# Performance work log

Hardware: AMD Instinct MI355X
Metric: run time of the kernel (lower is better)

## Reference

```python
import jax, jax.numpy as jnp
import numpy as np

FACTOR = 3   # ProbAttention factor hardcoded in Informer.__init__
N_HEADS = 8


def _ln(x, g, b, eps=1e-5):
    m = x.mean(-1, keepdims=True)
    v = ((x - m) ** 2).mean(-1, keepdims=True)
    return (x - m) / jnp.sqrt(v + eps) * g + b


def _pos_emb(L, d_model):
    # standard fixed sinusoidal positional embedding (Informer PositionalEmbedding)
    pos = np.arange(L, dtype=np.float32)[:, None]
    div = np.exp(np.arange(0, d_model, 2, dtype=np.float32) * (-np.log(10000.0) / d_model))
    pe = np.zeros((L, d_model), np.float32)
    pe[:, 0::2] = np.sin(pos * div)
    pe[:, 1::2] = np.cos(pos * div)
    return jnp.asarray(pe)


def _prob_attention(q, k, v, rng_key):
    # q,k,v: [B, L, H, D]; mask_flag=False, scale=None -> 1/sqrt(D)
    B, L, H, D = q.shape
    Q = q.transpose(0, 2, 1, 3)
    K = k.transpose(0, 2, 1, 3)
    V = v.transpose(0, 2, 1, 3)
    L_Q = L_K = L
    U_part = min(FACTOR * int(np.ceil(np.log(L_K))), L_K)   # sampled keys per query
    u = min(FACTOR * int(np.ceil(np.log(L_Q))), L_Q)        # top queries kept
    # sample keys (shared across batch/heads, as in torch.randint(L_K,(L_Q,sample_k)))
    idx_sample = jax.random.randint(rng_key, (L_Q, U_part), 0, L_K)
    K_sample = K[:, :, idx_sample, :]                        # [B,H,L_Q,U_part,D]
    QK_sample = jnp.einsum('bhld,bhlsd->bhls', Q, K_sample)  # [B,H,L_Q,U_part]
    M = QK_sample.max(-1) - QK_sample.sum(-1) / L_K          # sparsity measure [B,H,L_Q]
    _, idx_top = jax.lax.top_k(M, u)                         # [B,H,u]
    Q_reduce = jnp.take_along_axis(Q, idx_top[..., None], axis=2)          # [B,H,u,D]
    scores = jnp.einsum('bhud,bhkd->bhuk', Q_reduce, K) / jnp.sqrt(jnp.float32(D))
    attn = jax.nn.softmax(scores, axis=-1)
    upd = jnp.einsum('bhuk,bhkd->bhud', attn, V)             # [B,H,u,D]
    # initial context = mean over values (mask_flag=False), overwrite at top queries
    ctx = jnp.broadcast_to(V.mean(axis=2, keepdims=True), (B, H, L_Q, D))
    bI = jnp.arange(B)[:, None, None]
    hI = jnp.arange(H)[None, :, None]
    ctx = ctx.at[bI, hI, idx_top].set(upd)
    return ctx.transpose(0, 2, 1, 3).reshape(B, L, H * D)


def _forward(x, time_features, g_in, b_in, W_tok, W_time, b_time,
             Wq, bq, Wk, bk, Wv, bv, Wo, bo, W1, b1, W2, b2,
             g1, be1, g2, be2, g_enc, b_enc, W_pre, b_pre, W_fc, b_fc):
    B, L, _ = x.shape
    d_model = W_tok.shape[-1]
    H = N_HEADS
    D = d_model // H
    x = _ln(x, g_in, b_in)                                   # input_norm over enc_in
    # DataEmbedding: circular Conv1d(k=3) token emb + positional + timeF linear
    xp = jnp.pad(x, ((0, 0), (1, 1), (0, 0)), mode='wrap')
    tok = jax.lax.conv_general_dilated(xp, W_tok, (1,), 'VALID',
                                       dimension_numbers=('NWC', 'WIO', 'NWC'))
    h = tok + _pos_emb(L, d_model)[None] + time_features @ W_time.T + b_time
    key = jax.random.key(42)
    for i in range(Wq.shape[0]):                              # e_layers (small, fixed)
        q = (h @ Wq[i].T + bq[i]).reshape(B, L, H, D)
        k = (h @ Wk[i].T + bk[i]).reshape(B, L, H, D)
        v = (h @ Wv[i].T + bv[i]).reshape(B, L, H, D)
        attn_out = _prob_attention(q, k, v, jax.random.fold_in(key, i))
        h = h + attn_out @ Wo[i].T + bo[i]
        h = _ln(h, g1[i], be1[i])
        y = jax.nn.relu(h @ W1[i].T + b1[i]) @ W2[i].T + b2[i]  # 1x1 convs == linears
        h = _ln(h + y, g2[i], be2[i])
    h = _ln(h, g_enc, b_enc)
    last = h[:, -1, :]
    return jax.nn.relu(last @ W_pre.T + b_pre) @ W_fc.T + b_fc


def setup_inputs() -> dict:
    key = jax.random.key(0)
    B, L, C_IN, DM, DFF, E = 8, 2048, 32, 512, 2048, 2
    ks = iter(jax.random.split(key, 48))

    def p(shape, s=0.02):
        return jax.random.normal(next(ks), shape, jnp.float32) * s

    return {
        'x': jax.random.normal(next(ks), (B, L, C_IN), jnp.float32),
        'time_features': jax.random.uniform(next(ks), (B, L, 4), jnp.float32),
        'g_in': jnp.ones((C_IN,), jnp.float32), 'b_in': jnp.zeros((C_IN,), jnp.float32),
        'W_tok': p((3, C_IN, DM)),
        'W_time': p((DM, 4)), 'b_time': jnp.zeros((DM,), jnp.float32),
        'Wq': p((E, DM, DM)), 'bq': jnp.zeros((E, DM), jnp.float32),
        'Wk': p((E, DM, DM)), 'bk': jnp.zeros((E, DM), jnp.float32),
        'Wv': p((E, DM, DM)), 'bv': jnp.zeros((E, DM), jnp.float32),
        'Wo': p((E, DM, DM)), 'bo': jnp.zeros((E, DM), jnp.float32),
        'W1': p((E, DFF, DM)), 'b1': jnp.zeros((E, DFF), jnp.float32),
        'W2': p((E, DM, DFF)), 'b2': jnp.zeros((E, DM), jnp.float32),
        'g1': jnp.ones((E, DM), jnp.float32), 'be1': jnp.zeros((E, DM), jnp.float32),
        'g2': jnp.ones((E, DM), jnp.float32), 'be2': jnp.zeros((E, DM), jnp.float32),
        'g_enc': jnp.ones((DM,), jnp.float32), 'b_enc': jnp.zeros((DM,), jnp.float32),
        'W_pre': p((DM // 2, DM)), 'b_pre': jnp.zeros((DM // 2,), jnp.float32),
        'W_fc': p((1, DM // 2)), 'b_fc': jnp.zeros((1,), jnp.float32),
    }


def reference(x, time_features, g_in, b_in, W_tok, W_time, b_time,
              Wq, bq, Wk, bk, Wv, bv, Wo, bo, W1, b1, W2, b2,
              g1, be1, g2, be2, g_enc, b_enc, W_pre, b_pre, W_fc, b_fc):
    return _forward(x, time_features, g_in, b_in, W_tok, W_time, b_time,
                    Wq, bq, Wk, bk, Wv, bv, Wo, bo, W1, b1, W2, b2,
                    g1, be1, g2, be2, g_enc, b_enc, W_pre, b_pre, W_fc, b_fc)
```

## Files before the change

### kernel.cpp

```cpp
#include <hip/hip_runtime.h>
#include <math.h>

#define BATCH 8
#define SEQ   2048
#define TOK   (BATCH*SEQ)
#define CIN   32
#define DM    512
#define DFF   2048
#define NH    8
#define HD    64
#define NSAMP 24
#define NTOP  24
#define EPS   1e-5f
#define QKVLD 1536

typedef unsigned int u32;
typedef unsigned short u16;
typedef unsigned long long u64;
typedef __attribute__((ext_vector_type(8))) short short8;
typedef __attribute__((ext_vector_type(4))) short short4v;
typedef __attribute__((ext_vector_type(4))) float floatx4;

__device__ __forceinline__ void async16(const void* g, void* l) {
    __builtin_amdgcn_global_load_lds((const __attribute__((address_space(1))) u32*)g,
                                     (__attribute__((address_space(3))) u32*)l, 16, 0, 0);
}
__device__ __forceinline__ u16 bf16rn(float f) {
    u32 u = __float_as_uint(f);
    return (u16)((u + 0x7fffu + ((u >> 16) & 1u)) >> 16);
}
__device__ __forceinline__ void sep_store(u16* base, size_t row, int ld2, int j, float v) {
    u16 hb = bf16rn(v);
    float r = v - __uint_as_float((u32)hb << 16);
    size_t o = row * (size_t)ld2 + (size_t)((j >> 3) << 4) + (j & 7);
    base[o] = hb;
    base[o + 8] = bf16rn(r);
}
__device__ __forceinline__ float sep_load(const u16* base, size_t row, int ld2, int j) {
    size_t o = row * (size_t)ld2 + (size_t)((j >> 3) << 4) + (j & 7);
    return __uint_as_float((u32)base[o] << 16) + __uint_as_float((u32)base[o + 8] << 16);
}
__device__ __forceinline__ float hl2f(u16 h, u16 l) {
    return __uint_as_float((u32)h << 16) + __uint_as_float((u32)l << 16);
}

__device__ __forceinline__ void tf_round(unsigned &x0, unsigned &x1, int r) {
    x0 += x1;
    x1 = (x1 << r) | (x1 >> (32 - r));
    x1 ^= x0;
}
__device__ __forceinline__ void threefry(unsigned k0, unsigned k1,
                                         unsigned c0, unsigned c1,
                                         unsigned &o0, unsigned &o1) {
    unsigned ks0 = k0, ks1 = k1, ks2 = k0 ^ k1 ^ 0x1BD11BDAu;
    unsigned x0 = c0 + ks0, x1 = c1 + ks1;
    tf_round(x0,x1,13); tf_round(x0,x1,15); tf_round(x0,x1,26); tf_round(x0,x1,6);
    x0 += ks1; x1 += ks2 + 1u;
    tf_round(x0,x1,17); tf_round(x0,x1,29); tf_round(x0,x1,16); tf_round(x0,x1,24);
    x0 += ks2; x1 += ks0 + 2u;
    tf_round(x0,x1,13); tf_round(x0,x1,15); tf_round(x0,x1,26); tf_round(x0,x1,6);
    x0 += ks0; x1 += ks1 + 3u;
    tf_round(x0,x1,17); tf_round(x0,x1,29); tf_round(x0,x1,16); tf_round(x0,x1,24);
    x0 += ks1; x1 += ks2 + 4u;
    tf_round(x0,x1,13); tf_round(x0,x1,15); tf_round(x0,x1,26); tf_round(x0,x1,6);
    x0 += ks2; x1 += ks0 + 5u;
    o0 = x0; o1 = x1;
}

__global__ void sample_kernel(int* __restrict__ idx_sample) {
    const int HALF = (SEQ * NSAMP) / 2;
    int p = blockIdx.x * blockDim.x + threadIdx.x;
    int li = blockIdx.y;
    if (p >= HALF) return;
    unsigned f0, f1;
    threefry(0u, 42u, 0u, (unsigned)li, f0, f1);
    unsigned a0, a1, b0, b1;
    threefry(f0, f1, 0u, 2u, a0, a1);
    threefry(f0, f1, 1u, 3u, b0, b1);
    unsigned o0, o1;
    threefry(a1, b1, (unsigned)p, (unsigned)(p + HALF), o0, o1);
    idx_sample[li * SEQ * NSAMP + p]        = (int)(o0 & (SEQ - 1));
    idx_sample[li * SEQ * NSAMP + p + HALF] = (int)(o1 & (SEQ - 1));
}

__global__ __launch_bounds__(256) void ln_in_kernel(const float* __restrict__ x,
        const float* __restrict__ g, const float* __restrict__ b,
        float* __restrict__ out) {
    int t = blockIdx.x * blockDim.x + threadIdx.x;
    if (t >= TOK) return;
    const float* xr = x + (size_t)t * CIN;
    float vals[CIN];
    float s = 0.f;
#pragma unroll
    for (int c = 0; c < CIN; c++) { vals[c] = xr[c]; s += vals[c]; }
    float m = s * (1.f / CIN);
    float v = 0.f;
#pragma unroll
    for (int c = 0; c < CIN; c++) { float d = vals[c] - m; v += d * d; }
    v *= (1.f / CIN);
    float inv = rsqrtf(v + EPS);
    float* orow = out + (size_t)t * CIN;
#pragma unroll
    for (int c = 0; c < CIN; c++) orow[c] = (vals[c] - m) * inv * g[c] + b[c];
}

__global__ __launch_bounds__(128) void im2col_kernel(const float* __restrict__ xln,
        u16* __restrict__ a) {
    int t = blockIdx.x;
    int j = threadIdx.x;
    if (j >= 96) return;
    int b = t >> 11, l = t & 2047;
    int w = j >> 5, c = j & 31;
    int lw = (l - 1 + w + SEQ) & 2047;
    sep_store(a, (size_t)t, 192, j, xln[(((size_t)b << 11) | lw) * CIN + c]);
}

__global__ __launch_bounds__(256) void wtok_split(const float* __restrict__ Wtok,
        u16* __restrict__ wt) {
    int e = blockIdx.x * 256 + threadIdx.x;
    int o = e / 96, j = e % 96;
    sep_store(wt, (size_t)o, 192, j, Wtok[(size_t)j * DM + o]);
}

__global__ __launch_bounds__(256) void pe_kernel(float* __restrict__ pe) {
    int e = blockIdx.x * 256 + threadIdx.x;
    int l = e >> 9, o = e & 511;
    const float c1 = -0.017988946039016f;
    int i2 = o & ~1;
    float div = expf((float)i2 * c1);
    float arg = (float)l * div;
    pe[e] = (o & 1) ? cosf(arg) : sinf(arg);
}

__global__ __launch_bounds__(256) void rsd_kernel(const float* __restrict__ pe,
        const float* __restrict__ tfeat, const float* __restrict__ Wtime,
        u16* __restrict__ rsd) {
    int t = blockIdx.x, tid = threadIdx.x;
    int l = t & 2047;
    float t0 = tfeat[(size_t)t * 4], t1 = tfeat[(size_t)t * 4 + 1];
    float t2 = tfeat[(size_t)t * 4 + 2], t3 = tfeat[(size_t)t * 4 + 3];
    for (int o = tid; o < DM; o += 256) {
        float v = pe[l * DM + o]
            + t0 * Wtime[o * 4] + t1 * Wtime[o * 4 + 1]
            + t2 * Wtime[o * 4 + 2] + t3 * Wtime[o * 4 + 3];
        sep_store(rsd, (size_t)t, 1024, o, v);
    }
}

__global__ __launch_bounds__(256) void split_weights(const float* __restrict__ Wq,
        const float* __restrict__ Wk, const float* __restrict__ Wv,
        const float* __restrict__ Wo, const float* __restrict__ W1,
        const float* __restrict__ W2, u16* __restrict__ out,
        const float* __restrict__ bq, const float* __restrict__ bk,
        const float* __restrict__ bv, float* __restrict__ bqkv) {
    int i = blockIdx.x * 256 + threadIdx.x;
    if (i < 1536)
        bqkv[i] = (i < 512) ? bq[i] : (i < 1024) ? bk[i - 512] : bv[i - 1024];
    if (i < 1048576) {
        const float* src = (i < 262144) ? Wq : (i < 524288) ? Wk : (i < 786432) ? Wv : Wo;
        int off = i & 262143;
        size_t base = (size_t)(i >> 18) * 524288;
        sep_store(out + base, (size_t)(off >> 9), 1024, off & 511, src[off]);
    } else if (i < 2097152) {
        int off = i - 1048576;
        sep_store(out + 2097152, (size_t)(off >> 9), 1024, off & 511, W1[off]);
    } else {
        int off = i - 2097152;
        sep_store(out + 4194304, (size_t)(off >> 11), 4096, off & 2047, W2[off]);
    }
}

template<bool RELU, bool RESP, bool OUTP, bool OUTB>
__global__ __launch_bounds__(256, 2) void gemm_pp(const u16* __restrict__ Ap,
        const u16* __restrict__ Wp, const float* __restrict__ bias,
        const u16* __restrict__ RsdS, float* __restrict__ Cf, u16* __restrict__ Cp,
        int ldc, int K, int lda) {
    __shared__ alignas(16) u16 At[2][8192];
    __shared__ alignas(16) u16 Wt[2][8192];
    const int tid = threadIdx.x;
    int linear = blockIdx.y * gridDim.x + blockIdx.x;
    int xcd = linear & 7, sseq = linear >> 3;
    int mper = gridDim.y >> 3;
    int mt = xcd * mper + (sseq % mper);
    int nt = sseq / mper;
    const int m0 = mt * 128, n0 = nt * 128;
    const int lane = tid & 63, wv = tid >> 6;
    const int wm = wv >> 1, wn = wv & 1;
    const int fr = lane & 15, q = lane >> 4;

    floatx4 acc[4][4] = {};

    const int r0 = tid >> 3;
    const int gc = (tid & 7) ^ (r0 & 7);
    const u16* abase = Ap + (size_t)(m0 + r0) * (2 * lda) + gc * 8;
    const u16* wbase = Wp + (size_t)(n0 + r0) * (2 * K) + gc * 8;
    const size_t astep = (size_t)32 * 2 * lda;
    const size_t wstep = (size_t)32 * 2 * K;
    const int doff = tid * 16;
    const int nk = K >> 5;

    const int cph = ((q << 1) ^ (fr & 7)) << 3;
    const int cpl = ((q << 1) ^ (fr & 7) ^ 1) << 3;

#pragma unroll
    for (int i = 0; i < 4; i++) {
        async16(abase + i * astep, (char*)At[0] + doff + i * 4096);
        async16(wbase + i * wstep, (char*)Wt[0] + doff + i * 4096);
    }

    for (int k = 0; k < nk; k++) {
        const int b = k & 1;
        __syncthreads();
        if (k + 1 < nk) {
            int k2 = (k + 1) << 6;
#pragma unroll
            for (int i = 0; i < 4; i++) {
                async16(abase + k2 + i * astep, (char*)At[b ^ 1] + doff + i * 4096);
                async16(wbase + k2 + i * wstep, (char*)Wt[b ^ 1] + doff + i * 4096);
            }
        }
        short8 ah[4], al[4];
#pragma unroll
        for (int mi = 0; mi < 4; mi++) {
            int r = wm * 64 + mi * 16 + fr;
            ah[mi] = *(const short8*)&At[b][r * 64 + cph];
            al[mi] = *(const short8*)&At[b][r * 64 + cpl];
        }
#pragma unroll
        for (int ni = 0; ni < 4; ni++) {
            int r = wn * 64 + ni * 16 + fr;
            short8 wh8 = *(const short8*)&Wt[b][r * 64 + cph];
            short8 wl8 = *(const short8*)&Wt[b][r * 64 + cpl];
#pragma unroll
            for (int mi = 0; mi < 4; mi++) {
                acc[mi][ni] = __builtin_amdgcn_mfma_f32_16x16x32_bf16(ah[mi], wh8, acc[mi][ni], 0, 0, 0);
                acc[mi][ni] = __builtin_amdgcn_mfma_f32_16x16x32_bf16(ah[mi], wl8, acc[mi][ni], 0, 0, 0);
                acc[mi][ni] = __builtin_amdgcn_mfma_f32_16x16x32_bf16(al[mi], wh8, acc[mi][ni], 0, 0, 0);
            }
        }
    }
#pragma unroll
    for (int ni = 0; ni < 4; ni++) {
        int col = n0 + wn * 64 + ni * 16 + fr;
        float bv = bias[col];
#pragma unroll
        for (int mi = 0; mi < 4; mi++) {
            int row = m0 + wm * 64 + mi * 16 + q * 4;
#pragma unroll
            for (int r = 0; r < 4; r++) {
                float v = acc[mi][ni][r] + bv;
                if (RESP) v += sep_load(RsdS, (size_t)(row + r), 2 * ldc, col);
                if (RELU) v = fmaxf(v, 0.f);
                if (OUTP)      sep_store(Cp, (size_t)(row + r), 2 * ldc, col, v);
                else if (OUTB) Cp[(size_t)(row + r) * ldc + col] = bf16rn(v);
                else           Cf[(size_t)(row + r) * ldc + col] = v;
            }
        }
    }
}

template<int CFG, bool RELU, bool RESP, bool OUTP, bool OUTB>
__global__ __launch_bounds__(512, 2) void gemm8(const u16* __restrict__ Ap,
        const u16* __restrict__ Wp, const float* __restrict__ bias,
        const u16* __restrict__ RsdS, float* __restrict__ Cf, u16* __restrict__ Cp,
        int ldc, int K, int lda) {
    constexpr int BM = CFG ? 256 : 128;
    constexpr int BN = CFG ? 128 : 256;
    constexpr int NA = BM / 64;
    constexpr int NW = BN / 64;
    __shared__ alignas(16) u16 As[3][BM * 64];
    __shared__ alignas(16) u16 Ws[3][BN * 64];
    const int tid = threadIdx.x;
    int linear = blockIdx.y * gridDim.x + blockIdx.x;
    int xcd = linear & 7, sseq = linear >> 3;
    int mper = gridDim.y >> 3;
    int mt = xcd * mper + (sseq % mper);
    int nt = sseq / mper;
    const int m0 = mt * BM, n0 = nt * BN;
    const int lane = tid & 63, wv = tid >> 6;
    const int wm = CFG ? (wv >> 1) : (wv >> 2);
    const int wn = CFG ? (wv & 1) : (wv & 3);
    const int fr = lane & 15, q = lane >> 4;

    floatx4 acc[4][4] = {};

    const int r0 = tid >> 3;
    const int gc = (tid & 7) ^ (r0 & 7);
    const u16* abase = Ap + (size_t)(m0 + r0) * (2 * lda) + gc * 8;
    const u16* wbase = Wp + (size_t)(n0 + r0) * (2 * K) + gc * 8;
    const size_t astep = (size_t)64 * 2 * lda;
    const size_t wstep = (size_t)64 * 2 * K;
    const int doff = tid * 16;
    const int nk = K >> 5;

    const int cph = ((q << 1) ^ (fr & 7)) << 3;
    const int cpl = cph ^ 8;

#pragma unroll
    for (int i = 0; i < NA; i++) async16(abase + i * astep, (char*)As[0] + doff + i * 8192);
#pragma unroll
    for (int i = 0; i < NW; i++) async16(wbase + i * wstep, (char*)Ws[0] + doff + i * 8192);
#pragma unroll
    for (int i = 0; i < NA; i++) async16(abase + 64 + i * astep, (char*)As[1] + doff + i * 8192);
#pragma unroll
    for (int i = 0; i < NW; i++) async16(wbase + 64 + i * wstep, (char*)Ws[1] + doff + i * 8192);
    asm volatile("s_waitcnt vmcnt(6)" ::: "memory");
    __builtin_amdgcn_s_barrier();

    int cur = 0;
    for (int k = 0; k < nk; k++) {
        const u16* Ab = As[cur];
        const u16* Wb = Ws[cur];
        int nxt = cur + 2; if (nxt >= 3) nxt -= 3;
        const bool stage = (k + 2) < nk;
        const int ko = (k + 2) << 6;

        short8 ah[4], al[4];
#pragma unroll
        for (int mi = 0; mi < 4; mi++) {
            int r = wm * 64 + mi * 16 + fr;
            ah[mi] = *(const short8*)&Ab[r * 64 + cph];
            al[mi] = *(const short8*)&Ab[r * 64 + cpl];
        }
        short8 wh, wl;
        {
            int r = wn * 64 + fr;
            wh = *(const short8*)&Wb[r * 64 + cph];
            wl = *(const short8*)&Wb[r * 64 + cpl];
        }
        if (stage) {
#pragma unroll
            for (int i = 0; i < NA; i++)
                async16(abase + ko + i * astep, (char*)As[nxt] + doff + i * 8192);
        }
        __builtin_amdgcn_s_barrier();
        asm volatile("s_waitcnt lgkmcnt(0)" ::: "memory");
        __builtin_amdgcn_sched_barrier(0);
        __builtin_amdgcn_s_setprio(1);
#pragma unroll
        for (int mi = 0; mi < 4; mi++) {
            acc[mi][0] = __builtin_amdgcn_mfma_f32_16x16x32_bf16(ah[mi], wh, acc[mi][0], 0, 0, 0);
            acc[mi][0] = __builtin_amdgcn_mfma_f32_16x16x32_bf16(ah[mi], wl, acc[mi][0], 0, 0, 0);
            acc[mi][0] = __builtin_amdgcn_mfma_f32_16x16x32_bf16(al[mi], wh, acc[mi][0], 0, 0, 0);
        }
        __builtin_amdgcn_s_setprio(0);
        __builtin_amdgcn_s_barrier();

#pragma unroll
        for (int ni = 1; ni < 4; ni++) {
            int r = wn * 64 + ni * 16 + fr;
            wh = *(const short8*)&Wb[r * 64 + cph];
            wl = *(const short8*)&Wb[r * 64 + cpl];
            if (stage) {
                if (ni == 1) {
#pragma unroll
                    for (int i = 0; i < NW / 2; i++)
                        async16(wbase + ko + i * wstep, (char*)Ws[nxt] + doff + i * 8192);
                } else if (ni == 2) {
#pragma unroll
                    for (int i = NW / 2; i < NW; i++)
                        async16(wbase + ko + i * wstep, (char*)Ws[nxt] + doff + i * 8192);
                }
            }
            __builtin_amdgcn_s_barrier();
            asm volatile("s_waitcnt lgkmcnt(0)" ::: "memory");
            __builtin_amdgcn_sched_barrier(0);
            __builtin_amdgcn_s_setprio(1);
#pragma unroll
            for (int mi = 0; mi < 4; mi++) {
                acc[mi][ni] = __builtin_amdgcn_mfma_f32_16x16x32_bf16(ah[mi], wh, acc[mi][ni], 0, 0, 0);
                acc[mi][ni] = __builtin_amdgcn_mfma_f32_16x16x32_bf16(ah[mi], wl, acc[mi][ni], 0, 0, 0);
                acc[mi][ni] = __builtin_amdgcn_mfma_f32_16x16x32_bf16(al[mi], wh, acc[mi][ni], 0, 0, 0);
            }
            __builtin_amdgcn_s_setprio(0);
            __builtin_amdgcn_s_barrier();
        }

        if (k + 1 < nk) {
            if (k + 2 < nk) asm volatile("s_waitcnt vmcnt(6)" ::: "memory");
            else            asm volatile("s_waitcnt vmcnt(0)" ::: "memory");
            __builtin_amdgcn_s_barrier();
        }
        cur++; if (cur == 3) cur = 0;
    }

#pragma unroll
    for (int ni = 0; ni < 4; ni++) {
        int col = n0 + wn * 64 + ni * 16 + fr;
        float bv = bias[col];
#pragma unroll
        for (int mi = 0; mi < 4; mi++) {
            int row = m0 + wm * 64 + mi * 16 + q * 4;
#pragma unroll
            for (int r = 0; r < 4; r++) {
                float v = acc[mi][ni][r] + bv;
                if (RESP) v += sep_load(RsdS, (size_t)(row + r), 2 * ldc, col);
                if (RELU) v = fmaxf(v, 0.f);
                if (OUTP)      sep_store(Cp, (size_t)(row + r), 2 * ldc, col, v);
                else if (OUTB) Cp[(size_t)(row + r) * ldc + col] = bf16rn(v);
                else           Cf[(size_t)(row + r) * ldc + col] = v;
            }
        }
    }
}

template<bool RELU, bool RESP>
__global__ __launch_bounds__(256, 2) void gemm_sb(const u16* __restrict__ Ab,
        const u16* __restrict__ Wp, const float* __restrict__ bias,
        const u16* __restrict__ RsdS, float* __restrict__ Cf,
        int ldc, int K, int lda) {
    __shared__ alignas(16) u16 At[2][4096];
    __shared__ alignas(16) u16 Wt[2][8192];
    const int tid = threadIdx.x;
    int linear = blockIdx.y * gridDim.x + blockIdx.x;
    int xcd = linear & 7, sseq = linear >> 3;
    int mper = gridDim.y >> 3;
    int mt = xcd * mper + (sseq % mper);
    int nt = sseq / mper;
    const int m0 = mt * 128, n0 = nt * 128;
    const int lane = tid & 63, wv = tid >> 6;
    const int wm = wv >> 1, wn = wv & 1;
    const int fr = lane & 15, q = lane >> 4;

    floatx4 acc[4][4] = {};

    const int ar = tid & 127;
    const u16* abase = Ab + (size_t)(m0 + ar) * lda + (tid >> 7) * 8;
    const int adoff = tid * 16;
    const int r0 = tid >> 3;
    const int gc = (tid & 7) ^ (r0 & 7);
    const u16* wbase = Wp + (size_t)(n0 + r0) * (2 * K) + gc * 8;
    const size_t wstep = (size_t)32 * 2 * K;
    const int wdoff = tid * 16;
    const int nk = K >> 5;

    const int cph = ((q << 1) ^ (fr & 7)) << 3;
    const int cpl = ((q << 1) ^ (fr & 7) ^ 1) << 3;

#pragma unroll
    for (int i = 0; i < 2; i++)
        async16(abase + i * 16, (char*)At[0] + adoff + i * 4096);
#pragma unroll
    for (int i = 0; i < 4; i++)
        async16(wbase + i * wstep, (char*)Wt[0] + wdoff + i * 4096);

    for (int k = 0; k < nk; k++) {
        const int b = k & 1;
        __syncthreads();
        if (k + 1 < nk) {
            int ka = (k + 1) << 5;
            int kw = (k + 1) << 6;
#pragma unroll
            for (int i = 0; i < 2; i++)
                async16(abase + ka + i * 16, (char*)At[b ^ 1] + adoff + i * 4096);
#pragma unroll
            for (int i = 0; i < 4; i++)
                async16(wbase + kw + i * wstep, (char*)Wt[b ^ 1] + wdoff + i * 4096);
        }
        short8 af[4];
#pragma unroll
        for (int mi = 0; mi < 4; mi++) {
            int r = wm * 64 + mi * 16 + fr;
            af[mi] = *(const short8*)&At[b][q * 1024 + r * 8];
        }
#pragma unroll
        for (int ni = 0; ni < 4; ni++) {
            int r = wn * 64 + ni * 16 + fr;
            short8 wh8 = *(const short8*)&Wt[b][r * 64 + cph];
            short8 wl8 = *(const short8*)&Wt[b][r * 64 + cpl];
#pragma unroll
            for (int mi = 0; mi < 4; mi++) {
                acc[mi][ni] = __builtin_amdgcn_mfma_f32_16x16x32_bf16(af[mi], wh8, acc[mi][ni], 0, 0, 0);
                acc[mi][ni] = __builtin_amdgcn_mfma_f32_16x16x32_bf16(af[mi], wl8, acc[mi][ni], 0, 0, 0);
            }
        }
    }
#pragma unroll
    for (int ni = 0; ni < 4; ni++) {
        int col = n0 + wn * 64 + ni * 16 + fr;
        float bv = bias[col];
#pragma unroll
        for (int mi = 0; mi < 4; mi++) {
            int row = m0 + wm * 64 + mi * 16 + q * 4;
#pragma unroll
            for (int r = 0; r < 4; r++) {
                float v = acc[mi][ni][r] + bv;
                if (RESP) v += sep_load(RsdS, (size_t)(row + r), 2 * ldc, col);
                if (RELU) v = fmaxf(v, 0.f);
                Cf[(size_t)(row + r) * ldc + col] = v;
            }
        }
    }
}

__global__ __launch_bounds__(256) void qk_sample_kernel(const float* __restrict__ qkv,
        const int* __restrict__ idx_sample, float* __restrict__ Mout) {
    int r = (blockIdx.x * 256 + threadIdx.x) >> 6;
    int lane = threadIdx.x & 63;
    if (r >= BATCH * NH * SEQ) return;
    int b = r / (NH * SEQ);
    int head = (r / SEQ) % NH;
    int l = r % SEQ;
    int sidx = lane >> 4, dc = lane & 15;
    const float* qrow = qkv + ((size_t)(b * SEQ + l)) * QKVLD + head * HD + dc * 4;
    float4 qf = *(const float4*)qrow;
    int myidx = (lane < NSAMP) ? idx_sample[l * NSAMP + lane] : 0;
    const float* kbase = qkv + (size_t)b * SEQ * QKVLD + 512 + head * HD + dc * 4;
    int kidx[6];
#pragma unroll
    for (int p = 0; p < 6; p++) kidx[p] = __shfl(myidx, p * 4 + sidx);
    float4 kf[6];
#pragma unroll
    for (int p = 0; p < 6; p++) kf[p] = *(const float4*)(kbase + (size_t)kidx[p] * QKVLD);
    float mx = -INFINITY, sm = 0.f;
#pragma unroll
    for (int p = 0; p < 6; p++) {
        float part = qf.x * kf[p].x + qf.y * kf[p].y + qf.z * kf[p].z + qf.w * kf[p].w;
        part += __shfl_xor(part, 1);
        part += __shfl_xor(part, 2);
        part += __shfl_xor(part, 4);
        part += __shfl_xor(part, 8);
        mx = fmaxf(mx, part);
        sm += part;
    }
    mx = fmaxf(mx, __shfl_xor(mx, 16));
    mx = fmaxf(mx, __shfl_xor(mx, 32));
    sm += __shfl_xor(sm, 16);
    sm += __shfl_xor(sm, 32);
    if (lane == 0) Mout[r] = mx - sm * (1.f / SEQ);
}

__device__ __forceinline__ u64 pack_key(float v, int idx) {
    u32 u = __float_as_uint(v);
    u32 m = (u & 0x80000000u) ? ~u : (u | 0x80000000u);
    return ((u64)m << 32) | (u32)(~(u32)idx);
}

__global__ __launch_bounds__(256) void topk_part(const float* __restrict__ Mbuf,
        u64* __restrict__ cand) {
    __shared__ u64 wred[4];
    int bh = blockIdx.x, chunk = blockIdx.y;
    int tid = threadIdx.x, wv = tid >> 6, lane = tid & 63;
    int l = chunk * 256 + tid;
    u64 val = pack_key(Mbuf[(size_t)bh * SEQ + l], l);
    for (int it = 0; it < NTOP; it++) {
        u64 w = val;
#pragma unroll
        for (int off = 32; off > 0; off >>= 1) {
            u64 o = __shfl_xor(w, off);
            if (o > w) w = o;
        }
        if (lane == 0) wred[wv] = w;
        __syncthreads();
        u64 win = wred[0];
        if (wred[1] > win) win = wred[1];
        if (wred[2] > win) win = wred[2];
        if (wred[3] > win) win = wred[3];
        if (val == win) val = 0;
        if (tid == 0) cand[((size_t)bh * 8 + chunk) * NTOP + it] = win;
        __syncthreads();
    }
}

__global__ __launch_bounds__(256) void topk_merge(const u64* __restrict__ cand,
        int* __restrict__ idx_top) {
    __shared__ u64 wred[4];
    int bh = blockIdx.x;
    int tid = threadIdx.x, wv = tid >> 6, lane = tid & 63;
    u64 val = (tid < 8 * NTOP) ? cand[(size_t)bh * 8 * NTOP + tid] : 0;
    for (int it = 0; it < NTOP; it++) {
        u64 w = val;
#pragma unroll
        for (int off = 32; off > 0; off >>= 1) {
            u64 o = __shfl_xor(w, off);
            if (o > w) w = o;
        }
        if (lane == 0) wred[wv] = w;
        __syncthreads();
        u64 win = wred[0];
        if (wred[1] > win) win = wred[1];
        if (wred[2] > win) win = wred[2];
        if (wred[3] > win) win = wred[3];
        if (val == win) val = 0;
        if (tid == 0) idx_top[bh * NTOP + it] = (int)(~(u32)(win & 0xffffffffull) & (SEQ - 1));
        __syncthreads();
    }
}

__global__ __launch_bounds__(256) void vmean_kernel(const float* __restrict__ qkv,
        float* __restrict__ vmean) {
    __shared__ float red[256];
    int bh = blockIdx.x, slab = blockIdx.y;
    int b = bh >> 3, head = bh & 7;
    int seg = threadIdx.x >> 6, d = threadIdx.x & 63;
    int base_row = slab * 256 + seg * 64;
    float s = 0.f;
    for (int r = 0; r < 64; r++)
        s += qkv[((size_t)(b * SEQ + base_row + r)) * QKVLD + 1024 + head * HD + d];
    red[threadIdx.x] = s;
    __syncthreads();
    if (threadIdx.x < 128) red[threadIdx.x] += red[threadIdx.x + 128];
    __syncthreads();
    if (threadIdx.x < 64) {
        float t = red[threadIdx.x] + red[threadIdx.x + 64];
        atomicAdd(&vmean[bh * HD + d], t * (1.f / SEQ));
    }
}

__global__ void fillctx_kernel(const float* __restrict__ vmean, u16* __restrict__ out) {
    int e = blockIdx.x * 256 + threadIdx.x;
    int t = e >> 6, g = e & 63;
    const float* vm = vmean + ((((t >> 11) << 3) | (g >> 3)) << 6) + (g & 7) * 8;
    short8 hh, ll;
#pragma unroll
    for (int s = 0; s < 8; s++) {
        float v = vm[s];
        u16 hb = bf16rn(v);
        hh[s] = (short)hb;
        ll[s] = (short)bf16rn(v - __uint_as_float((u32)hb << 16));
    }
    u16* dp = out + (size_t)t * 1024 + g * 16;
    *(short8*)dp = hh;
    *(short8*)(dp + 8) = ll;
}

__global__ __launch_bounds__(256) void spattn_flash(const float* __restrict__ qkv,
        const int* __restrict__ idx_top, float* __restrict__ opart,
        float* __restrict__ mspart) {
    __shared__ float KtT[64][65];
    __shared__ float Vt[64][65];
    __shared__ float Qs[24][64];
    __shared__ float Ps[24][66];
    int bh = blockIdx.x, slab = blockIdx.y;
    int b = bh >> 3, h = bh & 7;
    int tid = threadIdx.x;
    int wv = tid >> 6, lane = tid & 63;
    for (int i = tid; i < NTOP * 64; i += 256) {
        int u = i >> 6, d = i & 63;
        int qi = idx_top[bh * NTOP + u];
        Qs[u][d] = qkv[((size_t)(b * SEQ + qi)) * QKVLD + h * HD + d];
    }
    float m[6], s[6], o[6], alpha[6];
#pragma unroll
    for (int j = 0; j < 6; j++) { m[j] = -INFINITY; s[j] = 0.f; o[j] = 0.f; }
    int key0 = slab * 512;
    int sr = tid >> 2, sc0 = (tid & 3) * 16;
    for (int t = 0; t < 8; t++) {
        int kbase = key0 + t * 64;
        __syncthreads();
        const float* kr = qkv + ((size_t)(b * SEQ + kbase + sr)) * QKVLD + 512 + h * HD + sc0;
        const float* vr = qkv + ((size_t)(b * SEQ + kbase + sr)) * QKVLD + 1024 + h * HD + sc0;
        float kf[16], vf[16];
        *(float4*)&kf[0]  = *(const float4*)(kr);
        *(float4*)&kf[4]  = *(const float4*)(kr + 4);
        *(float4*)&kf[8]  = *(const float4*)(kr + 8);
        *(float4*)&kf[12] = *(const float4*)(kr + 12);
        *(float4*)&vf[0]  = *(const float4*)(vr);
        *(float4*)&vf[4]  = *(const float4*)(vr + 4);
        *(float4*)&vf[8]  = *(const float4*)(vr + 8);
        *(float4*)&vf[12] = *(const float4*)(vr + 12);
#pragma unroll
        for (int i = 0; i < 16; i++) {
            KtT[sc0 + i][sr] = kf[i];
            Vt[sr][sc0 + i] = vf[i];
        }
        __syncthreads();
        float dot[6] = {};
#pragma unroll
        for (int d = 0; d < 64; d++) {
            float kv = KtT[d][lane];
#pragma unroll
            for (int j = 0; j < 6; j++) dot[j] += Qs[wv * 6 + j][d] * kv;
        }
#pragma unroll
        for (int j = 0; j < 6; j++) {
            float sc = dot[j] * 0.125f;
            float tmax = sc;
            for (int off = 32; off > 0; off >>= 1) tmax = fmaxf(tmax, __shfl_xor(tmax, off));
            float mn = fmaxf(m[j], tmax);
            float p = __expf(sc - mn);
            float psum = p;
            for (int off = 32; off > 0; off >>= 1) psum += __shfl_xor(psum, off);
            alpha[j] = __expf(m[j] - mn);
            s[j] = s[j] * alpha[j] + psum;
            m[j] = mn;
            Ps[wv * 6 + j][lane] = p;
        }
        float pv[6] = {};
#pragma unroll
        for (int key = 0; key < 64; key++) {
            float vvv = Vt[key][lane];
#pragma unroll
            for (int j = 0; j < 6; j++) pv[j] += Ps[wv * 6 + j][key] * vvv;
        }
#pragma unroll
        for (int j = 0; j < 6; j++) o[j] = o[j] * alpha[j] + pv[j];
    }
    float* ob = opart + ((size_t)(bh * 4 + slab)) * NTOP * 64;
#pragma unroll
    for (int j = 0; j < 6; j++) ob[(wv * 6 + j) * 64 + lane] = o[j];
    if (lane == 0) {
        float* ms = mspart + ((size_t)(bh * 4 + slab)) * NTOP * 2;
#pragma unroll
        for (int j = 0; j < 6; j++) {
            ms[(wv * 6 + j) * 2]     = m[j];
            ms[(wv * 6 + j) * 2 + 1] = s[j];
        }
    }
}

__global__ __launch_bounds__(256) void spattn_combine(const float* __restrict__ opart,
        const float* __restrict__ mspart, const int* __restrict__ idx_top,
        u16* __restrict__ out) {
    __shared__ float wgt[4][NTOP];
    int bh = blockIdx.x;
    int b = bh >> 3, h = bh & 7;
    int tid = threadIdx.x;
    if (tid < NTOP) {
        float mv[4], sv[4];
        float M = -INFINITY;
#pragma unroll
        for (int sl = 0; sl < 4; sl++) {
            mv[sl] = mspart[((size_t)(bh * 4 + sl)) * NTOP * 2 + tid * 2];
            sv[sl] = mspart[((size_t)(bh * 4 + sl)) * NTOP * 2 + tid * 2 + 1];
            M = fmaxf(M, mv[sl]);
        }
        float S = 0.f;
#pragma unroll
        for (int sl = 0; sl < 4; sl++) S += sv[sl] * __expf(mv[sl] - M);
        float invS = 1.f / S;
#pragma unroll
        for (int sl = 0; sl < 4; sl++) wgt[sl][tid] = __expf(mv[sl] - M) * invS;
    }
    __syncthreads();
    for (int i = tid; i < NTOP * 64; i += 256) {
        int u = i >> 6, d = i & 63;
        float val = 0.f;
#pragma unroll
        for (int sl = 0; sl < 4; sl++)
            val += wgt[sl][u] * opart[(((size_t)(bh * 4 + sl)) * NTOP + u) * 64 + d];
        int qi = idx_top[bh * NTOP + u];
        sep_store(out, (size_t)(b * SEQ + qi), 1024, h * HD + d, val);
    }
}

template<bool INP, bool OUTSEP>
__global__ __launch_bounds__(256) void ln_kernel(const float* __restrict__ srcF,
        const u16* __restrict__ srcS, const float* __restrict__ g,
        const float* __restrict__ b, float* __restrict__ dstF, u16* __restrict__ dstS) {
    int wv = threadIdx.x >> 6, lane = threadIdx.x & 63;
    int t = blockIdx.x * 4 + wv;
    float xv[8];
    if (INP) {
        const u16* sp = srcS + (size_t)t * 1024 + (lane >> 1) * 16 + (lane & 1) * 4;
        short4v h0 = *(const short4v*)sp;
        short4v l0 = *(const short4v*)(sp + 8);
        short4v h1 = *(const short4v*)(sp + 512);
        short4v l1 = *(const short4v*)(sp + 520);
#pragma unroll
        for (int i = 0; i < 4; i++) {
            xv[i]     = hl2f((u16)h0[i], (u16)l0[i]);
            xv[i + 4] = hl2f((u16)h1[i], (u16)l1[i]);
        }
    } else {
        float4 x0 = *(const float4*)&srcF[(size_t)t * DM + lane * 4];
        float4 x1 = *(const float4*)&srcF[(size_t)t * DM + lane * 4 + 256];
        xv[0] = x0.x; xv[1] = x0.y; xv[2] = x0.z; xv[3] = x0.w;
        xv[4] = x1.x; xv[5] = x1.y; xv[6] = x1.z; xv[7] = x1.w;
    }
    float s = 0.f, s2 = 0.f;
#pragma unroll
    for (int i = 0; i < 8; i++) { s += xv[i]; s2 += xv[i] * xv[i]; }
#pragma unroll
    for (int off = 32; off > 0; off >>= 1) {
        s  += __shfl_xor(s, off);
        s2 += __shfl_xor(s2, off);
    }
    float m = s * (1.f / DM);
    float var = s2 * (1.f / DM) - m * m;
    float inv = rsqrtf(var + EPS);
    float4 g0 = *(const float4*)&g[lane * 4];
    float4 g1 = *(const float4*)&g[lane * 4 + 256];
    float4 b0 = *(const float4*)&b[lane * 4];
    float4 b1 = *(const float4*)&b[lane * 4 + 256];
    float y[8];
    y[0] = (xv[0] - m) * inv * g0.x + b0.x;  y[1] = (xv[1] - m) * inv * g0.y + b0.y;
    y[2] = (xv[2] - m) * inv * g0.z + b0.z;  y[3] = (xv[3] - m) * inv * g0.w + b0.w;
    y[4] = (xv[4] - m) * inv * g1.x + b1.x;  y[5] = (xv[5] - m) * inv * g1.y + b1.y;
    y[6] = (xv[6] - m) * inv * g1.z + b1.z;  y[7] = (xv[7] - m) * inv * g1.w + b1.w;
    if (OUTSEP) {
        u16* dp = dstS + (size_t)t * 1024 + (lane >> 1) * 16 + (lane & 1) * 4;
        short4v hh0, ll0, hh1, ll1;
#pragma unroll
        for (int i = 0; i < 4; i++) {
            u16 hb = bf16rn(y[i]);
            hh0[i] = (short)hb;
            ll0[i] = (short)bf16rn(y[i] - __uint_as_float((u32)hb << 16));
            u16 hb2 = bf16rn(y[i + 4]);
            hh1[i] = (short)hb2;
            ll1[i] = (short)bf16rn(y[i + 4] - __uint_as_float((u32)hb2 << 16));
        }
        *(short4v*)dp = hh0;
        *(short4v*)(dp + 8) = ll0;
        *(short4v*)(dp + 512) = hh1;
        *(short4v*)(dp + 520) = ll1;
    } else {
        float4 o0 = { y[0], y[1], y[2], y[3] };
        float4 o1 = { y[4], y[5], y[6], y[7] };
        *(float4*)&dstF[(size_t)t * DM + lane * 4] = o0;
        *(float4*)&dstF[(size_t)t * DM + lane * 4 + 256] = o1;
    }
}

__global__ __launch_bounds__(256) void head_kernel(const float* __restrict__ hfin,
        const float* __restrict__ Wpre, const float* __restrict__ bpre,
        const float* __restrict__ Wfc, const float* __restrict__ bfc,
        float* __restrict__ out) {
    __shared__ float last[DM];
    __shared__ float red[256];
    int b = blockIdx.x, tid = threadIdx.x;
    const float* hr = hfin + ((size_t)(b * SEQ + SEQ - 1)) * DM;
    last[tid] = hr[tid];
    last[tid + 256] = hr[tid + 256];
    __syncthreads();
    float acc = bpre[tid];
    for (int c = 0; c < DM; c++) acc += last[c] * Wpre[tid * DM + c];
    acc = fmaxf(acc, 0.f);
    red[tid] = acc * Wfc[tid];
    __syncthreads();
    for (int s = 128; s > 0; s >>= 1) { if (tid < s) red[tid] += red[tid + s]; __syncthreads(); }
    if (tid == 0) out[b] = red[0] + bfc[0];
}

extern "C" void kernel_launch(void* const* d_in, const int* in_sizes, int n_in,
                              void* d_out, int out_size, void* d_ws, size_t ws_size,
                              hipStream_t stream) {
    (void)in_sizes; (void)n_in; (void)out_size; (void)ws_size;
    const float* x      = (const float*)d_in[0];
    const float* tfeat  = (const float*)d_in[1];
    const float* g_in   = (const float*)d_in[2];
    const float* b_in   = (const float*)d_in[3];
    const float* W_tok  = (const float*)d_in[4];
    const float* W_time = (const float*)d_in[5];
    const float* b_time = (const float*)d_in[6];
    const float* Wq     = (const float*)d_in[7];
    const float* bq     = (const float*)d_in[8];
    const float* Wk     = (const float*)d_in[9];
    const float* bk     = (const float*)d_in[10];
    const float* Wv     = (const float*)d_in[11];
    const float* bv     = (const float*)d_in[12];
    const float* Wo     = (const float*)d_in[13];
    const float* bo     = (const float*)d_in[14];
    const float* W1     = (const float*)d_in[15];
    const float* b1     = (const float*)d_in[16];
    const float* W2     = (const float*)d_in[17];
    const float* b2     = (const float*)d_in[18];
    const float* g1     = (const float*)d_in[19];
    const float* be1    = (const float*)d_in[20];
    const float* g2     = (const float*)d_in[21];
    const float* be2    = (const float*)d_in[22];
    const float* g_enc  = (const float*)d_in[23];
    const float* b_enc  = (const float*)d_in[24];
    const float* W_pre  = (const float*)d_in[25];
    const float* b_pre  = (const float*)d_in[26];
    const float* W_fc   = (const float*)d_in[27];
    const float* b_fc   = (const float*)d_in[28];
    float* out = (float*)d_out;

    char* ws = (char*)d_ws;
    u16*   hp   = (u16*)(ws);
    float* hf   = (float*)(ws + 33554432);
    char*  bigc = ws + 67108864;
    float* qkv  = (float*)bigc;
    u16*   ctxP = (u16*)(bigc + 100663296);
    u16*   midP = (u16*)bigc;
    u16*   midB = (u16*)bigc;
    float* xln  = (float*)(bigc);
    u16*   acvP = (u16*)(bigc + 2097152);
    float* pe   = (float*)(bigc + 8388608);
    u16*   rsdS = (u16*)(bigc + 12582912);
    u16*   wtok = (u16*)(bigc + 46137344);
    u16*   wsep       = (u16*)(ws + 201326592);
    float* Mbuf       = (float*)(ws + 213909504);
    float* vmean      = (float*)(ws + 214433792);
    int*   idx_sample = (int*)(ws + 214450176);
    int*   idx_top    = (int*)(ws + 214843392);
    float* biasqkv    = (float*)(ws + 214849536);
    u64*   cand       = (u64*)(ws + 214855680);
    float* opart      = (float*)(ws + 214953984);
    float* mspart     = (float*)(ws + 216526848);

    ln_in_kernel<<<TOK / 256, 256, 0, stream>>>(x, g_in, b_in, xln);
    im2col_kernel<<<TOK, 128, 0, stream>>>(xln, acvP);
    wtok_split<<<192, 256, 0, stream>>>(W_tok, wtok);
    pe_kernel<<<4096, 256, 0, stream>>>(pe);
    rsd_kernel<<<TOK, 256, 0, stream>>>(pe, tfeat, W_time, rsdS);
    sample_kernel<<<dim3(96, 2), 256, 0, stream>>>(idx_sample);

    gemm_pp<false, true, true, false><<<dim3(4, 128), 256, 0, stream>>>(
        acvP, wtok, b_time, rsdS, nullptr, hp, DM, 96, 96);

    const u16* wqkv_p = wsep;
    const u16* wo_p = wsep + 1572864;
    const u16* w1_p = wsep + 2097152;
    const u16* w2_p = wsep + 4194304;

    for (int li = 0; li < 2; li++) {
        split_weights<<<12288, 256, 0, stream>>>(
            Wq + (size_t)li * DM * DM, Wk + (size_t)li * DM * DM,
            Wv + (size_t)li * DM * DM, Wo + (size_t)li * DM * DM,
            W1 + (size_t)li * DFF * DM, W2 + (size_t)li * DM * DFF, wsep,
            bq + (size_t)li * DM, bk + (size_t)li * DM, bv + (size_t)li * DM, biasqkv);

        const float* bo_i = bo + (size_t)li * DM;
        const float* b1_i = b1 + (size_t)li * DFF;
        const float* b2_i = b2 + (size_t)li * DM;
        const float* g1_i = g1 + (size_t)li * DM;
        const float* be1_i = be1 + (size_t)li * DM;
        const float* g2_i = g2 + (size_t)li * DM;
        const float* be2_i = be2 + (size_t)li * DM;

        gemm8<0, false, false, false, false><<<dim3(QKVLD / 256, TOK / 128), 512, 0, stream>>>(
            hp, wqkv_p, biasqkv, nullptr, qkv, nullptr, QKVLD, DM, DM);

        qk_sample_kernel<<<(BATCH * NH * SEQ) / 4, 256, 0, stream>>>(
            qkv, idx_sample + li * SEQ * NSAMP, Mbuf);
        topk_part<<<dim3(BATCH * NH, 8), 256, 0, stream>>>(Mbuf, cand);
        topk_merge<<<BATCH * NH, 256, 0, stream>>>(cand, idx_top);
        hipMemsetAsync(vmean, 0, BATCH * NH * HD * sizeof(float), stream);
        vmean_kernel<<<dim3(BATCH * NH, 8), 256, 0, stream>>>(qkv, vmean);
        fillctx_kernel<<<(TOK * 64) / 256, 256, 0, stream>>>(vmean, ctxP);
        spattn_flash<<<dim3(BATCH * NH, 4), 256, 0, stream>>>(qkv, idx_top, opart, mspart);
        spattn_combine<<<BATCH * NH, 256, 0, stream>>>(opart, mspart, idx_top, ctxP);

        gemm8<1, false, true, false, false><<<dim3(DM / 128, TOK / 256), 512, 0, stream>>>(
            ctxP, wo_p, bo_i, hp, hf, nullptr, DM, DM, DM);
        ln_kernel<false, true><<<TOK / 4, 256, 0, stream>>>(hf, nullptr, g1_i, be1_i, nullptr, hp);

        if (li == 0) {
            gemm8<0, true, false, true, false><<<dim3(DFF / 256, TOK / 128), 512, 0, stream>>>(
                hp, w1_p, b1_i, nullptr, nullptr, midP, DFF, DM, DM);
            gemm8<1, false, true, false, false><<<dim3(DM / 128, TOK / 256), 512, 0, stream>>>(
                midP, w2_p, b2_i, hp, hf, nullptr, DM, DFF, DFF);
        } else {
            gemm8<0, true, false, false, true><<<dim3(DFF / 256, TOK / 128), 512, 0, stream>>>(
                hp, w1_p, b1_i, nullptr, nullptr, midB, DFF, DM, DM);
            gemm_sb<false, true><<<dim3(DM / 128, TOK / 128), 256, 0, stream>>>(
                midB, w2_p, b2_i, hp, hf, DM, DFF, DFF);
        }
        ln_kernel<false, true><<<TOK / 4, 256, 0, stream>>>(hf, nullptr, g2_i, be2_i, nullptr, hp);
    }

    ln_kernel<true, false><<<TOK / 4, 256, 0, stream>>>(nullptr, hp, g_enc, b_enc, hf, nullptr);
    head_kernel<<<BATCH, 256, 0, stream>>>(hf, W_pre, b_pre, W_fc, b_fc, out);
}
```

Measured before the change: 1.267 ms.

## Simplify gemm main loop: issue all prefetches upfront, drop intra-iteration barriers

Rewrites the K-loop of the split-bf16 GEMM so that all async global->LDS loads for stage k+2 are issued at the top of the iteration. The per-N-subtile barriers, setprio and sched_barrier scheduling that interleaved LDS reads, prefetch issues and MFMA groups are removed, and the kernel is renamed. This cuts barrier overhead and lets the compiler schedule MFMAs freely. It also gives up the hand-tuned interleaving that hid memory issue latency behind compute and avoided contention among the two co-resident blocks.

```diff
diff --git a/kernel.cpp b/kernel.cpp
--- a/kernel.cpp
+++ b/kernel.cpp
@@ -260,7 +260,7 @@
 }
 
 template<int CFG, bool RELU, bool RESP, bool OUTP, bool OUTB>
-__global__ __launch_bounds__(512, 2) void gemm8(const u16* __restrict__ Ap,
+__global__ __launch_bounds__(512, 2) void gemm1p(const u16* __restrict__ Ap,
         const u16* __restrict__ Wp, const float* __restrict__ bias,
         const u16* __restrict__ RsdS, float* __restrict__ Cf, u16* __restrict__ Cp,
         int ldc, int K, int lda) {
@@ -312,8 +312,16 @@
         const u16* Ab = As[cur];
         const u16* Wb = Ws[cur];
         int nxt = cur + 2; if (nxt >= 3) nxt -= 3;
-        const bool stage = (k + 2) < nk;
-        const int ko = (k + 2) << 6;
+
+        if (k + 2 < nk) {
+            int ko = (k + 2) << 6;
+#pragma unroll
+            for (int i = 0; i < NA; i++)
+                async16(abase + ko + i * astep, (char*)As[nxt] + doff + i * 8192);
+#pragma unroll
+            for (int i = 0; i < NW; i++)
+                async16(wbase + ko + i * wstep, (char*)Ws[nxt] + doff + i * 8192);
+        }
 
         short8 ah[4], al[4];
 #pragma unroll
@@ -322,58 +330,17 @@
             ah[mi] = *(const short8*)&Ab[r * 64 + cph];
             al[mi] = *(const short8*)&Ab[r * 64 + cpl];
         }
-        short8 wh, wl;
-        {
-            int r = wn * 64 + fr;
-            wh = *(const short8*)&Wb[r * 64 + cph];
-            wl = *(const short8*)&Wb[r * 64 + cpl];
-        }
-        if (stage) {
-#pragma unroll
-            for (int i = 0; i < NA; i++)
-                async16(abase + ko + i * astep, (char*)As[nxt] + doff + i * 8192);
-        }
-        __builtin_amdgcn_s_barrier();
-        asm volatile("s_waitcnt lgkmcnt(0)" ::: "memory");
-        __builtin_amdgcn_sched_barrier(0);
-        __builtin_amdgcn_s_setprio(1);
-#pragma unroll
-        for (int mi = 0; mi < 4; mi++) {
-            acc[mi][0] = __builtin_amdgcn_mfma_f32_16x16x32_bf16(ah[mi], wh, acc[mi][0], 0, 0, 0);
-            acc[mi][0] = __builtin_amdgcn_mfma_f32_16x16x32_bf16(ah[mi], wl, acc[mi][0], 0, 0, 0);
-            acc[mi][0] = __builtin_amdgcn_mfma_f32_16x16x32_bf16(al[mi], wh, acc[mi][0], 0, 0, 0);
-        }
-        __builtin_amdgcn_s_setprio(0);
-        __builtin_amdgcn_s_barrier();
-
-#pragma unroll
-        for (int ni = 1; ni < 4; ni++) {
+#pragma unroll
+        for (int ni = 0; ni < 4; ni++) {
             int r = wn * 64 + ni * 16 + fr;
-            wh = *(const short8*)&Wb[r * 64 + cph];
-            wl = *(const short8*)&Wb[r * 64 + cpl];
-            if (stage) {
-                if (ni == 1) {
-#pragma unroll
-                    for (int i = 0; i < NW / 2; i++)
-                        async16(wbase + ko + i * wstep, (char*)Ws[nxt] + doff + i * 8192);
-                } else if (ni == 2) {
-#pragma unroll
-                    for (int i = NW / 2; i < NW; i++)
-                        async16(wbase + ko + i * wstep, (char*)Ws[nxt] + doff + i * 8192);
-                }
+            short8 wh8 = *(const short8*)&Wb[r * 64 + cph];
+            short8 wl8 = *(const short8*)&Wb[r * 64 + cpl];
+#pragma unroll
+            for (int mi = 0; mi < 4; mi++) {
+                acc[mi][ni] = __builtin_amdgcn_mfma_f32_16x16x32_bf16(ah[mi], wh8, acc[mi][ni], 0, 0, 0);
+                acc[mi][ni] = __builtin_amdgcn_mfma_f32_16x16x32_bf16(ah[mi], wl8, acc[mi][ni], 0, 0, 0);
+                acc[mi][ni] = __builtin_amdgcn_mfma_f32_16x16x32_bf16(al[mi], wh8, acc[mi][ni], 0, 0, 0);
             }
-            __builtin_amdgcn_s_barrier();
-            asm volatile("s_waitcnt lgkmcnt(0)" ::: "memory");
-            __builtin_amdgcn_sched_barrier(0);
-            __builtin_amdgcn_s_setprio(1);
-#pragma unroll
-            for (int mi = 0; mi < 4; mi++) {
-                acc[mi][ni] = __builtin_amdgcn_mfma_f32_16x16x32_bf16(ah[mi], wh, acc[mi][ni], 0, 0, 0);
-                acc[mi][ni] = __builtin_amdgcn_mfma_f32_16x16x32_bf16(ah[mi], wl, acc[mi][ni], 0, 0, 0);
-                acc[mi][ni] = __builtin_amdgcn_mfma_f32_16x16x32_bf16(al[mi], wh, acc[mi][ni], 0, 0, 0);
-            }
-            __builtin_amdgcn_s_setprio(0);
-            __builtin_amdgcn_s_barrier();
         }
 
         if (k + 1 < nk) {
@@ -920,7 +887,7 @@
         const float* g2_i = g2 + (size_t)li * DM;
         const float* be2_i = be2 + (size_t)li * DM;
 
-        gemm8<0, false, false, false, false><<<dim3(QKVLD / 256, TOK / 128), 512, 0, stream>>>(
+        gemm1p<0, false, false, false, false><<<dim3(QKVLD / 256, TOK / 128), 512, 0, stream>>>(
             hp, wqkv_p, biasqkv, nullptr, qkv, nullptr, QKVLD, DM, DM);
 
         qk_sample_kernel<<<(BATCH * NH * SEQ) / 4, 256, 0, stream>>>(
@@ -933,17 +900,17 @@
         spattn_flash<<<dim3(BATCH * NH, 4), 256, 0, stream>>>(qkv, idx_top, opart, mspart);
         spattn_combine<<<BATCH * NH, 256, 0, stream>>>(opart, mspart, idx_top, ctxP);
 
-        gemm8<1, false, true, false, false><<<dim3(DM / 128, TOK / 256), 512, 0, stream>>>(
+        gemm1p<1, false, true, false, false><<<dim3(DM / 128, TOK / 256), 512, 0, stream>>>(
             ctxP, wo_p, bo_i, hp, hf, nullptr, DM, DM, DM);
         ln_kernel<false, true><<<TOK / 4, 256, 0, stream>>>(hf, nullptr, g1_i, be1_i, nullptr, hp);
 
         if (li == 0) {
-            gemm8<0, true, false, true, false><<<dim3(DFF / 256, TOK / 128), 512, 0, stream>>>(
+            gemm1p<0, true, false, true, false><<<dim3(DFF / 256, TOK / 128), 512, 0, stream>>>(
                 hp, w1_p, b1_i, nullptr, nullptr, midP, DFF, DM, DM);
-            gemm8<1, false, true, false, false><<<dim3(DM / 128, TOK / 256), 512, 0, stream>>>(
+            gemm1p<1, false, true, false, false><<<dim3(DM / 128, TOK / 256), 512, 0, stream>>>(
                 midP, w2_p, b2_i, hp, hf, nullptr, DM, DFF, DFF);
         } else {
-            gemm8<0, true, false, false, true><<<dim3(DFF / 256, TOK / 128), 512, 0, stream>>>(
+            gemm1p<0, true, false, false, true><<<dim3(DFF / 256, TOK / 128), 512, 0, stream>>>(
                 hp, w1_p, b1_i, nullptr, nullptr, midB, DFF, DM, DM);
             gemm_sb<false, true><<<dim3(DM / 128, TOK / 128), 256, 0, stream>>>(
                 midB, w2_p, b2_i, hp, hf, DM, DFF, DFF);
```

New measurement: 1.249 ms. No clear change (-1.4%).
